# Kernel optimization log

Measured on AMD Instinct MI355X. Metric: run time of the kernel, lower is better.

## Reference

```python
import jax, jax.numpy as jnp
import numpy as np

B, S, D = 8, 2048, 512          # batch, seq_len, latent_doc_dim
E = 512                          # embedding_dim (== latent_doc_dim here by construction)
NUM_CATS, NUM_LABELS = 1024, 8192
EMB_SCALING = 1.0


def _norm_embed(m, scaling):
    # __init__ preprocessing: m -= m.mean(); m /= m.std() * scaling
    m = m - m.mean()
    return m / (m.std() * scaling)


def setup_inputs() -> dict:
    key = jax.random.key(0)
    k1, k2, k3, k4, k5, k6, k7 = jax.random.split(key, 7)
    K = jax.random.normal(k1, (B, S, D), dtype=jnp.float32)
    V = jax.random.normal(k2, (B, S, D), dtype=jnp.float32)
    code2cat_map = jax.random.randint(k3, (NUM_LABELS,), 0, NUM_CATS)
    # pretrained embedding matrices, normalized as in __init__
    Q1_w = _norm_embed(jax.random.normal(k4, (NUM_CATS, E), dtype=jnp.float32), EMB_SCALING)
    Q2_w = _norm_embed(jax.random.normal(k5, (NUM_LABELS, E), dtype=jnp.float32), EMB_SCALING)
    # Conv1d(kernel_size=1): weight [D_out=latent, D_in=embed], bias [latent]
    map_w = jax.random.normal(k6, (D, E), dtype=jnp.float32) / np.sqrt(E)
    map_b = jax.random.normal(k7, (D,), dtype=jnp.float32) * 0.01
    return {"K": K, "V": V, "code2cat_map": code2cat_map,
            "Q1_w": Q1_w, "Q2_w": Q2_w, "map_w": map_w, "map_b": map_b}


def reference(K, V, code2cat_map, Q1_w, Q2_w, map_w, map_b):
    # kernel-size-1 Conv1d mapping == affine projection of each row embedding
    Q1 = jnp.einsum('ce,de->cd', Q1_w, map_w) + map_b        # [num_cats, D]
    Q2 = jnp.einsum('le,de->ld', Q2_w, map_w) + map_b        # [num_labels, D]
    # level-1 attention (scale=False)
    E1 = jnp.einsum('cd,bsd->bcs', Q1, K)                    # [B, num_cats, S]
    A1 = jax.nn.softmax(E1, axis=-1)
    C1 = jnp.einsum('bcs,bsd->bcd', A1, V)                   # [B, num_cats, D]
    # inject level-1 context into level-2 queries via code->category gather-add
    Q2b = Q2[None, :, :] + C1[:, code2cat_map, :]            # [B, num_labels, D]
    # level-2 attention
    E2 = jnp.einsum('bld,bsd->bls', Q2b, K)                  # [B, num_labels, S]
    A2 = jax.nn.softmax(E2, axis=-1)
    C2 = jnp.einsum('bls,bsd->bld', A2, V)                   # [B, num_labels, D]
    return (C2, E2)
```

## Files before the change

### kernel.cpp

```cpp
#include <hip/hip_runtime.h>
#include <hip/hip_bf16.h>
#include <stdint.h>

#define BB 8
#define SS 2048
#define DD 512
#define NCAT 1024
#define NLAB 8192

typedef short bf16x8 __attribute__((ext_vector_type(8)));
typedef short bf16x4_t __attribute__((ext_vector_type(4)));
typedef float f32x4 __attribute__((ext_vector_type(4)));

#define BAR() do { asm volatile("" ::: "memory"); __builtin_amdgcn_s_barrier(); asm volatile("" ::: "memory"); } while (0)

__device__ __forceinline__ unsigned short f2bf(float f) {
  union { float f; unsigned int u; } v; v.f = f;
  unsigned int u = v.u;
  return (unsigned short)((u + 0x7fffu + ((u >> 16) & 1u)) >> 16);
}
__device__ __forceinline__ float bf2f(unsigned short h) {
  union { unsigned int u; float f; } v; v.u = ((unsigned int)h) << 16;
  return v.f;
}

__device__ __forceinline__ void gload_lds16(const void* g, void* l) {
  __builtin_amdgcn_global_load_lds(
      (const __attribute__((address_space(1))) unsigned int*)g,
      (__attribute__((address_space(3))) unsigned int*)l, 16, 0, 0);
}

__global__ __launch_bounds__(512, 2) void gemm_e2(
    const short* __restrict__ A,
    const short* __restrict__ Bm,
    float* __restrict__ E2, float* __restrict__ pm, float* __restrict__ ps)
{
  __shared__ __align__(16) char lds[3 * 32768];
  const int t = threadIdx.x;
  const int w = t >> 6, lane = t & 63;
  const int r = lane & 15, g = lane >> 4;
  const int wm = w >> 2, wn = w & 3;
  const int m0 = blockIdx.x * 256, n0 = blockIdx.y * 256;
  const int b = blockIdx.z;
  const short* Ab = A + (long)b * NLAB * DD;
  const short* Bb = Bm + (long)b * SS * DD;

  int offA[8], offB[4];
#pragma unroll
  for (int i = 0; i < 8; ++i) {
    int row = wm * 128 + i * 16 + r;
    int grp = row >> 1, slot = ((row & 1) << 2) | g;
    offA[i] = grp * 128 + (slot ^ (grp & 7)) * 16;
  }
#pragma unroll
  for (int j = 0; j < 4; ++j) {
    int row = wn * 64 + j * 16 + r;
    int grp = row >> 1, slot = ((row & 1) << 2) | g;
    offB[j] = grp * 128 + (slot ^ (grp & 7)) * 16;
  }

  int srow[2], scol[2];
#pragma unroll
  for (int ld = 0; ld < 2; ++ld) {
    int ch = ld * 512 + t;
    int grp = ch >> 3, sl2 = (ch & 7) ^ (grp & 7);
    srow[ld] = grp * 2 + (sl2 >> 2);
    scol[ld] = (sl2 & 3) * 8;
  }

  auto stageA = [&](int kt, int buf) {
    const long kb = (long)(kt * 32);
#pragma unroll
    for (int ld = 0; ld < 2; ++ld)
      gload_lds16(Ab + (long)(m0 + srow[ld]) * DD + kb + scol[ld],
                  lds + buf * 32768 + (ld * 512 + t) * 16);
  };
  auto stageB = [&](int kt, int buf) {
    const long kb = (long)(kt * 32);
#pragma unroll
    for (int ld = 0; ld < 2; ++ld)
      gload_lds16(Bb + (long)(n0 + srow[ld]) * DD + kb + scol[ld],
                  lds + buf * 32768 + 16384 + (ld * 512 + t) * 16);
  };

  f32x4 acc[8][4] = {};

  stageA(0, 0); stageB(0, 0);
  stageA(1, 1); stageB(1, 1);
  asm volatile("s_waitcnt vmcnt(4)" ::: "memory");
  BAR();

  int cur = 0;
#pragma unroll 1
  for (int kt = 0; kt < 16; ++kt) {
    const char* bA = lds + cur * 32768;
    const char* bB = bA + 16384;
    const int nxt = (cur == 0) ? 2 : cur - 1;

    bf16x8 av[4], av2[4], bv[4];
#pragma unroll
    for (int j = 0; j < 4; ++j) bv[j] = *(const bf16x8*)(bB + offB[j]);
#pragma unroll
    for (int i = 0; i < 4; ++i) av[i] = *(const bf16x8*)(bA + offA[i]);
    if (kt + 2 < 16) stageA(kt + 2, nxt);
    BAR();
    __builtin_amdgcn_s_setprio(1);
#pragma unroll
    for (int i = 0; i < 4; ++i)
#pragma unroll
      for (int j = 0; j < 4; ++j)
        acc[i][j] = __builtin_amdgcn_mfma_f32_16x16x32_bf16(av[i], bv[j], acc[i][j], 0, 0, 0);
    __builtin_amdgcn_s_setprio(0);
    BAR();
#pragma unroll
    for (int i = 0; i < 4; ++i) av2[i] = *(const bf16x8*)(bA + offA[4 + i]);
    if (kt + 2 < 16) stageB(kt + 2, nxt);
    BAR();
    __builtin_amdgcn_s_setprio(1);
#pragma unroll
    for (int i = 0; i < 4; ++i)
#pragma unroll
      for (int j = 0; j < 4; ++j)
        acc[4 + i][j] = __builtin_amdgcn_mfma_f32_16x16x32_bf16(av2[i], bv[j], acc[4 + i][j], 0, 0, 0);
    __builtin_amdgcn_s_setprio(0);
    if (kt < 15) {
      if (kt == 14) asm volatile("s_waitcnt vmcnt(0)" ::: "memory");
      else          asm volatile("s_waitcnt vmcnt(4)" ::: "memory");
    }
    BAR();
    cur = (cur == 2) ? 0 : cur + 1;
  }

  float* Cg = E2 + (long)b * NLAB * SS;
#pragma unroll
  for (int i = 0; i < 8; ++i)
#pragma unroll
    for (int j = 0; j < 4; ++j) {
      const int col = n0 + wn * 64 + j * 16 + r;
#pragma unroll
      for (int q = 0; q < 4; ++q) {
        const int row = m0 + wm * 128 + i * 16 + g * 4 + q;
        Cg[(long)row * SS + col] = acc[i][j][q];
      }
    }

  BAR();

  float* smax = (float*)lds;
  float* ssum = (float*)(lds + 4096);
#pragma unroll
  for (int i = 0; i < 8; ++i)
#pragma unroll
    for (int q = 0; q < 4; ++q) {
      float mm = fmaxf(fmaxf(acc[i][0][q], acc[i][1][q]),
                       fmaxf(acc[i][2][q], acc[i][3][q]));
#pragma unroll
      for (int off = 1; off <= 8; off <<= 1) mm = fmaxf(mm, __shfl_xor(mm, off, 64));
      float s = 0.f;
#pragma unroll
      for (int j = 0; j < 4; ++j) s += __expf(acc[i][j][q] - mm);
#pragma unroll
      for (int off = 1; off <= 8; off <<= 1) s += __shfl_xor(s, off, 64);
      if (r == 0) {
        const int rowt = wm * 128 + i * 16 + g * 4 + q;
        smax[rowt * 4 + wn] = mm;
        ssum[rowt * 4 + wn] = s;
      }
    }
  BAR();
  if (t < 256) {
    float m0_ = smax[t * 4 + 0], m1_ = smax[t * 4 + 1];
    float m2_ = smax[t * 4 + 2], m3_ = smax[t * 4 + 3];
    float mm = fmaxf(fmaxf(m0_, m1_), fmaxf(m2_, m3_));
    float s = ssum[t * 4 + 0] * __expf(m0_ - mm) + ssum[t * 4 + 1] * __expf(m1_ - mm)
            + ssum[t * 4 + 2] * __expf(m2_ - mm) + ssum[t * 4 + 3] * __expf(m3_ - mm);
    const long base = ((long)b * NLAB + m0 + t) * 8 + (n0 >> 8);
    pm[base] = mm;
    ps[base] = s;
  }
}

__global__ __launch_bounds__(512, 2) void gemm_c2p(
    const float* __restrict__ E2, const float2* __restrict__ stats,
    const short* __restrict__ VT, float* __restrict__ C2)
{
  __shared__ __align__(16) char lds[3 * 32768];
  const int t = threadIdx.x;
  const int w = t >> 6, lane = t & 63;
  const int r = lane & 15, g = lane >> 4;
  const int wm = w >> 2, wn = w & 3;
  const int m0 = blockIdx.x * 256, n0 = blockIdx.y * 256;
  const int b = blockIdx.z;
  const float* Eb = E2 + (long)b * NLAB * SS;
  const short* Bb = VT + (long)b * DD * SS;

  int offA[8], offB[4];
#pragma unroll
  for (int i = 0; i < 8; ++i) {
    int row = wm * 128 + i * 16 + r;
    int grp = row >> 1, slot = ((row & 1) << 2) | g;
    offA[i] = grp * 128 + (slot ^ (grp & 7)) * 16;
  }
#pragma unroll
  for (int j = 0; j < 4; ++j) {
    int row = wn * 64 + j * 16 + r;
    int grp = row >> 1, slot = ((row & 1) << 2) | g;
    offB[j] = grp * 128 + (slot ^ (grp & 7)) * 16;
  }

  int srow[2], scol[2];
#pragma unroll
  for (int ld = 0; ld < 2; ++ld) {
    int ch = ld * 512 + t;
    int grp = ch >> 3, sl2 = (ch & 7) ^ (grp & 7);
    srow[ld] = grp * 2 + (sl2 >> 2);
    scol[ld] = (sl2 & 3) * 8;
  }

  const int arow = t >> 1;
  const int ac0 = (t & 1) * 16;
  int wbyte[2];
  {
    const int grp = arow >> 1, cc0 = ac0 >> 3;
#pragma unroll
    for (int ld = 0; ld < 2; ++ld) {
      const int slot = ((arow & 1) << 2) | (cc0 + ld);
      wbyte[ld] = grp * 128 + (slot ^ (grp & 7)) * 16;
    }
  }
  const float2 st = stats[(long)b * NLAB + m0 + arow];
  const float* asrc = Eb + (long)(m0 + arow) * SS + ac0;

  float areg[16];
  auto loadA = [&](int kt) {
    const float* src = asrc + kt * 32;
#pragma unroll
    for (int u = 0; u < 4; ++u)
      *(f32x4*)(areg + u * 4) = *(const f32x4*)(src + u * 4);
  };
  auto writeA = [&](int buf) {
    char* dst = lds + buf * 32768;
#pragma unroll
    for (int ld = 0; ld < 2; ++ld) {
      bf16x8 p;
#pragma unroll
      for (int q = 0; q < 8; ++q)
        p[q] = (short)f2bf(__expf(areg[ld * 8 + q] - st.x) * st.y);
      *(bf16x8*)(dst + wbyte[ld]) = p;
    }
  };
  auto stageB = [&](int kt, int buf) {
    const long kb = (long)(kt * 32);
#pragma unroll
    for (int ld = 0; ld < 2; ++ld)
      gload_lds16(Bb + (long)(n0 + srow[ld]) * SS + kb + scol[ld],
                  lds + buf * 32768 + 16384 + (ld * 512 + t) * 16);
  };

  f32x4 acc[8][4] = {};

  loadA(0); stageB(0, 0); writeA(0);
  loadA(1); stageB(1, 1); writeA(1);
  asm volatile("s_waitcnt lgkmcnt(0)" ::: "memory");
  BAR();

  int cur = 0;
#pragma unroll 1
  for (int kt = 0; kt < 64; ++kt) {
    const char* bA = lds + cur * 32768;
    const char* bB = bA + 16384;
    const int nxt = (cur == 0) ? 2 : cur - 1;

    bf16x8 av[4], av2[4], bv[4];
#pragma unroll
    for (int j = 0; j < 4; ++j) bv[j] = *(const bf16x8*)(bB + offB[j]);
#pragma unroll
    for (int i = 0; i < 4; ++i) av[i] = *(const bf16x8*)(bA + offA[i]);
    if (kt + 2 < 64) loadA(kt + 2);
    BAR();
    __builtin_amdgcn_s_setprio(1);
#pragma unroll
    for (int i = 0; i < 4; ++i)
#pragma unroll
      for (int j = 0; j < 4; ++j)
        acc[i][j] = __builtin_amdgcn_mfma_f32_16x16x32_bf16(av[i], bv[j], acc[i][j], 0, 0, 0);
    __builtin_amdgcn_s_setprio(0);
    BAR();
#pragma unroll
    for (int i = 0; i < 4; ++i) av2[i] = *(const bf16x8*)(bA + offA[4 + i]);
    if (kt + 2 < 64) stageB(kt + 2, nxt);
    BAR();
    __builtin_amdgcn_s_setprio(1);
#pragma unroll
    for (int i = 0; i < 4; ++i)
#pragma unroll
      for (int j = 0; j < 4; ++j)
        acc[4 + i][j] = __builtin_amdgcn_mfma_f32_16x16x32_bf16(av2[i], bv[j], acc[4 + i][j], 0, 0, 0);
    __builtin_amdgcn_s_setprio(0);
    if (kt + 2 < 64) writeA(nxt);
    if (kt == 62) asm volatile("s_waitcnt vmcnt(0)" ::: "memory");
    asm volatile("s_waitcnt lgkmcnt(0)" ::: "memory");
    BAR();
    cur = (cur == 2) ? 0 : cur + 1;
  }

  float* Cg = C2 + (long)b * NLAB * DD;
#pragma unroll
  for (int i = 0; i < 8; ++i)
#pragma unroll
    for (int j = 0; j < 4; ++j) {
      const int col = n0 + wn * 64 + j * 16 + r;
#pragma unroll
      for (int q = 0; q < 4; ++q) {
        const int row = m0 + wm * 128 + i * 16 + g * 4 + q;
        Cg[(long)row * DD + col] = acc[i][j][q];
      }
    }
}

template<int BIAS, int TERMS>
__global__ __launch_bounds__(256) void gemm_nt_split(
    const short* __restrict__ Ah, const short* __restrict__ Al,
    const short* __restrict__ Bh, const short* __restrict__ Bl,
    float* __restrict__ C, const float* __restrict__ bias,
    int M, int N, int K, long sA, long sB, long sC)
{
  __shared__ short AsH[128 * 32];
  __shared__ short AsL[TERMS == 3 ? 128 * 32 : 8];
  __shared__ short BsH[128 * 32];
  __shared__ short BsL[TERMS == 3 ? 128 * 32 : 8];
  const int t = threadIdx.x, w = t >> 6, l = t & 63;
  const int r = l & 15, g = l >> 4;
  const int m0 = blockIdx.x * 128, n0 = blockIdx.y * 128;
  const int b = blockIdx.z;
  const short* Ahb = Ah + (long)b * sA;
  const short* Alb = TERMS == 3 ? Al + (long)b * sA : (const short*)0;
  const short* Bhb = Bh + (long)b * sB;
  const short* Blb = TERMS == 3 ? Bl + (long)b * sB : (const short*)0;
  float* Cg = C + (long)b * sC;
  const int wm = (w >> 1) * 64, wn = (w & 1) * 64;
  const int srow = t >> 2, scol = (t & 3) * 8;

  f32x4 acc[4][4] = {};

  const int nk = K >> 5;
  for (int kt = 0; kt < nk; ++kt) {
    const long k0 = (long)(kt << 5);
    const long ga0 = (long)(m0 + srow) * K + k0 + scol;
    const long ga1 = (long)(m0 + srow + 64) * K + k0 + scol;
    const long gb0 = (long)(n0 + srow) * K + k0 + scol;
    const long gb1 = (long)(n0 + srow + 64) * K + k0 + scol;
    gload_lds16(Ahb + ga0, &AsH[w * 512]);
    gload_lds16(Ahb + ga1, &AsH[2048 + w * 512]);
    gload_lds16(Bhb + gb0, &BsH[w * 512]);
    gload_lds16(Bhb + gb1, &BsH[2048 + w * 512]);
    if (TERMS == 3) {
      gload_lds16(Alb + ga0, &AsL[w * 512]);
      gload_lds16(Alb + ga1, &AsL[2048 + w * 512]);
      gload_lds16(Blb + gb0, &BsL[w * 512]);
      gload_lds16(Blb + gb1, &BsL[2048 + w * 512]);
    }
    __syncthreads();
    bf16x8 ah[4], al_[4], bh[4], bl_[4];
#pragma unroll
    for (int i = 0; i < 4; ++i) {
      ah[i]  = *(const bf16x8*)&AsH[(wm + i * 16 + r) * 32 + g * 8];
      bh[i]  = *(const bf16x8*)&BsH[(wn + i * 16 + r) * 32 + g * 8];
      if (TERMS == 3) {
        al_[i] = *(const bf16x8*)&AsL[(wm + i * 16 + r) * 32 + g * 8];
        bl_[i] = *(const bf16x8*)&BsL[(wn + i * 16 + r) * 32 + g * 8];
      }
    }
#pragma unroll
    for (int i = 0; i < 4; ++i)
#pragma unroll
      for (int j = 0; j < 4; ++j) {
        if (TERMS == 3) {
          acc[i][j] = __builtin_amdgcn_mfma_f32_16x16x32_bf16(al_[i], bh[j], acc[i][j], 0, 0, 0);
          acc[i][j] = __builtin_amdgcn_mfma_f32_16x16x32_bf16(ah[i], bl_[j], acc[i][j], 0, 0, 0);
        }
        acc[i][j] = __builtin_amdgcn_mfma_f32_16x16x32_bf16(ah[i], bh[j], acc[i][j], 0, 0, 0);
      }
    __syncthreads();
  }

#pragma unroll
  for (int i = 0; i < 4; ++i)
#pragma unroll
    for (int j = 0; j < 4; ++j) {
      f32x4 v = acc[i][j];
      const int col = n0 + wn + j * 16 + r;
      float bv = 0.f;
      if (BIAS) bv = bias[col];
#pragma unroll
      for (int q = 0; q < 4; ++q) {
        const int row = m0 + wm + i * 16 + g * 4 + q;
        Cg[(long)row * N + col] = v[q] + bv;
      }
    }
}

__global__ __launch_bounds__(256) void stats_combine(
    const float* __restrict__ pm, const float* __restrict__ ps,
    float2* __restrict__ stats)
{
  const long row = (long)blockIdx.x * 256 + threadIdx.x;
  const float* m = pm + row * 8;
  const float* s = ps + row * 8;
  float mv[8];
  float mm = -3.4e38f;
#pragma unroll
  for (int j = 0; j < 8; ++j) { mv[j] = m[j]; mm = fmaxf(mm, mv[j]); }
  float ss = 0.f;
#pragma unroll
  for (int j = 0; j < 8; ++j) ss += s[j] * __expf(mv[j] - mm);
  stats[row] = make_float2(mm, 1.f / ss);
}

__global__ __launch_bounds__(256) void rowsoft_p(
    const float* __restrict__ X, short* __restrict__ Ph)
{
  __shared__ float red[8];
  const long row = blockIdx.x;
  const float* x = X + row * SS;
  const int t = threadIdx.x, w = t >> 6;
  f32x4 v0 = *(const f32x4*)(x + t * 4);
  f32x4 v1 = *(const f32x4*)(x + 1024 + t * 4);
  float m = fmaxf(fmaxf(fmaxf(v0[0], v0[1]), fmaxf(v0[2], v0[3])),
                  fmaxf(fmaxf(v1[0], v1[1]), fmaxf(v1[2], v1[3])));
#pragma unroll
  for (int off = 32; off; off >>= 1) m = fmaxf(m, __shfl_xor(m, off, 64));
  if ((t & 63) == 0) red[w] = m;
  __syncthreads();
  m = fmaxf(fmaxf(red[0], red[1]), fmaxf(red[2], red[3]));
  float s = 0.f;
#pragma unroll
  for (int i = 0; i < 4; ++i) { v0[i] = __expf(v0[i] - m); s += v0[i]; }
#pragma unroll
  for (int i = 0; i < 4; ++i) { v1[i] = __expf(v1[i] - m); s += v1[i]; }
#pragma unroll
  for (int off = 32; off; off >>= 1) s += __shfl_xor(s, off, 64);
  if ((t & 63) == 0) red[4 + w] = s;
  __syncthreads();
  s = red[4] + red[5] + red[6] + red[7];
  const float inv = 1.f / s;
  bf16x4_t h0, h1;
#pragma unroll
  for (int i = 0; i < 4; ++i) {
    h0[i] = (short)f2bf(v0[i] * inv);
    h1[i] = (short)f2bf(v1[i] * inv);
  }
  *(bf16x4_t*)(Ph + row * SS + t * 4) = h0;
  *(bf16x4_t*)(Ph + row * SS + 1024 + t * 4) = h1;
}

__global__ __launch_bounds__(256) void cvt_split(
    const float* __restrict__ in, short* __restrict__ hi, short* __restrict__ lo, long n4)
{
  long i = (long)blockIdx.x * 256 + threadIdx.x;
  const long stride = (long)gridDim.x * 256;
  for (; i < n4; i += stride) {
    f32x4 v = *(const f32x4*)(in + i * 4);
    bf16x4_t h, lw;
#pragma unroll
    for (int q = 0; q < 4; ++q) {
      h[q] = (short)f2bf(v[q]);
      lw[q] = (short)f2bf(v[q] - bf2f((unsigned short)h[q]));
    }
    *(bf16x4_t*)(hi + i * 4) = h;
    *(bf16x4_t*)(lo + i * 4) = lw;
  }
}

__global__ __launch_bounds__(256) void vtrans(
    const float* __restrict__ V, short* __restrict__ TH)
{
  __shared__ float tile[32][33];
  const int b = blockIdx.z;
  const int s0 = blockIdx.x * 32, d0 = blockIdx.y * 32;
  const int tx = threadIdx.x & 31, ty = threadIdx.x >> 5;
  const float* Vb = V + (long)b * SS * DD;
  short* Hb = TH + (long)b * DD * SS;
#pragma unroll
  for (int i = 0; i < 32; i += 8)
    tile[ty + i][tx] = Vb[(long)(s0 + ty + i) * DD + d0 + tx];
  __syncthreads();
#pragma unroll
  for (int i = 0; i < 32; i += 8)
    Hb[(long)(d0 + ty + i) * SS + s0 + tx] = (short)f2bf(tile[tx][ty + i]);
}

__global__ __launch_bounds__(256) void make_q2b(
    const float* __restrict__ Q2f, const float* __restrict__ C1,
    const int* __restrict__ map, short* __restrict__ Oh)
{
  const long idx = (long)blockIdx.x * 256 + threadIdx.x;
  const long per_b = (long)NLAB * (DD / 4);
  const int b = (int)(idx / per_b);
  const long rem = idx - (long)b * per_b;
  const int ll = (int)(rem >> 7);
  const int dd = (int)(rem & 127) << 2;
  const int cat = map[ll];
  f32x4 qv = *(const f32x4*)(Q2f + (long)ll * DD + dd);
  f32x4 cv = *(const f32x4*)(C1 + ((long)b * NCAT + cat) * DD + dd);
  bf16x4_t h;
#pragma unroll
  for (int q = 0; q < 4; ++q) h[q] = (short)f2bf(qv[q] + cv[q]);
  *(bf16x4_t*)(Oh + idx * 4) = h;
}

extern "C" void kernel_launch(void* const* d_in, const int* in_sizes, int n_in,
                              void* d_out, int out_size, void* d_ws, size_t ws_size,
                              hipStream_t stream)
{
  const float* K    = (const float*)d_in[0];
  const float* V    = (const float*)d_in[1];
  const int*   map  = (const int*)d_in[2];
  const float* Q1w  = (const float*)d_in[3];
  const float* Q2w  = (const float*)d_in[4];
  const float* mapw = (const float*)d_in[5];
  const float* mapb = (const float*)d_in[6];

  float* out = (float*)d_out;
  const long C2SZ = (long)BB * NLAB * DD;
  float* outC2 = out;
  float* outE2 = out + C2SZ;

  char* ws = (char*)d_ws;
  short* Kh   = (short*)ws; ws += (long)BB * SS * DD * 2;
  short* Kl   = (short*)ws; ws += (long)BB * SS * DD * 2;
  short* VTh  = (short*)ws; ws += (long)BB * DD * SS * 2;
  short* Qwh  = (short*)ws; ws += (long)(NCAT + NLAB) * DD * 2;
  short* Qwl  = (short*)ws; ws += (long)(NCAT + NLAB) * DD * 2;
  short* mwh  = (short*)ws; ws += (long)DD * DD * 2;
  short* mwl  = (short*)ws; ws += (long)DD * DD * 2;
  float* Qall = (float*)ws; ws += (long)(NCAT + NLAB) * DD * 4;
  short* A1h  = (short*)ws; ws += (long)BB * NCAT * SS * 2;
  float* C1   = (float*)ws; ws += (long)BB * NCAT * DD * 4;
  short* Q2bh = (short*)ws; ws += (long)BB * NLAB * DD * 2;
  float* pm   = (float*)ws; ws += (long)BB * NLAB * 8 * 4;
  float* psum = (float*)ws; ws += (long)BB * NLAB * 8 * 4;
  float2* stats = (float2*)ws;

  cvt_split<<<2048, 256, 0, stream>>>(K, Kh, Kl, (long)BB * SS * DD / 4);
  vtrans<<<dim3(SS / 32, DD / 32, BB), 256, 0, stream>>>(V, VTh);
  cvt_split<<<512, 256, 0, stream>>>(Q1w, Qwh, Qwl, (long)NCAT * DD / 4);
  cvt_split<<<2048, 256, 0, stream>>>(Q2w, Qwh + (long)NCAT * DD, Qwl + (long)NCAT * DD,
                                      (long)NLAB * DD / 4);
  cvt_split<<<256, 256, 0, stream>>>(mapw, mwh, mwl, (long)DD * DD / 4);

  gemm_nt_split<1, 3><<<dim3((NCAT + NLAB) / 128, DD / 128, 1), 256, 0, stream>>>(
      Qwh, Qwl, mwh, mwl, Qall, mapb, NCAT + NLAB, DD, DD, 0, 0, 0);

  cvt_split<<<2048, 256, 0, stream>>>(Qall, Qwh, Qwl, (long)(NCAT + NLAB) * DD / 4);

  gemm_nt_split<0, 3><<<dim3(NCAT / 128, SS / 128, BB), 256, 0, stream>>>(
      Qwh, Qwl, Kh, Kl, outE2, (const float*)0,
      NCAT, SS, DD, 0, (long)SS * DD, (long)NCAT * SS);

  rowsoft_p<<<BB * NCAT, 256, 0, stream>>>(outE2, A1h);

  gemm_nt_split<0, 1><<<dim3(NCAT / 128, DD / 128, BB), 256, 0, stream>>>(
      A1h, (const short*)0, VTh, (const short*)0, C1, (const float*)0,
      NCAT, DD, SS, (long)NCAT * SS, (long)DD * SS, (long)NCAT * DD);

  make_q2b<<<(int)((long)BB * NLAB * DD / 4 / 256), 256, 0, stream>>>(
      Qall + (long)NCAT * DD, C1, map, Q2bh);

  gemm_e2<<<dim3(NLAB / 256, SS / 256, BB), 512, 0, stream>>>(
      Q2bh, Kh, outE2, pm, psum);

  stats_combine<<<BB * NLAB / 256, 256, 0, stream>>>(pm, psum, stats);

  gemm_c2p<<<dim3(NLAB / 256, DD / 256, BB), 512, 0, stream>>>(
      outE2, stats, VTh, outC2);
}
```

Measured before the change: 794.8 us.

## Reuse tuned QK and PV kernels for level-1 attention via concatenated split-bf16 operands

Level-1 attention now uses the pipelined 256x256 gemm_qk and gemm_pv kernels. The 3-term split-bf16 product is expressed as a single GEMM with K=1536 over concatenated [Qh|Ql|Qh] and [Kh|Kl|Kh] operands. The separate Qall split-conversion pass and the rowsoft_p kernel are removed. Softmax stats are fused into the QK epilogue and normalization into the PV kernel, and the Q1 split is written straight from the projection GEMM epilogue. This trades extra Kcat workspace and conversion writes for fewer launches, no materialized A1, and better-tuned GEMMs.

```diff
diff --git a/kernel.cpp b/kernel.cpp
--- a/kernel.cpp
+++ b/kernel.cpp
@@ -30,11 +30,15 @@
       (__attribute__((address_space(3))) unsigned int*)l, 16, 0, 0);
 }
 
-__global__ __launch_bounds__(512, 2) void gemm_e2(
-    const short* __restrict__ A,
-    const short* __restrict__ Bm,
-    float* __restrict__ E2, float* __restrict__ pm, float* __restrict__ ps)
-{
+template<int KK>
+__global__ __launch_bounds__(512, 2) void gemm_qk(
+    const short* __restrict__ A, long sA,
+    const short* __restrict__ Bc,
+    float* __restrict__ E, float* __restrict__ pm, float* __restrict__ ps,
+    int M)
+{
+  constexpr int NK = KK / 32;
+  constexpr int AS = (KK == 512) ? 512 : 1024;
   __shared__ __align__(16) char lds[3 * 32768];
   const int t = threadIdx.x;
   const int w = t >> 6, lane = t & 63;
@@ -42,8 +46,8 @@
   const int wm = w >> 2, wn = w & 3;
   const int m0 = blockIdx.x * 256, n0 = blockIdx.y * 256;
   const int b = blockIdx.z;
-  const short* Ab = A + (long)b * NLAB * DD;
-  const short* Bb = Bm + (long)b * SS * DD;
+  const short* Ab = A + (long)b * sA;
+  const short* Bb = Bc + (long)b * SS * KK;
 
   int offA[8], offB[4];
 #pragma unroll
@@ -69,17 +73,18 @@
   }
 
   auto stageA = [&](int kt, int buf) {
-    const long kb = (long)(kt * 32);
+    const int ab = (KK == 512) ? kt : (kt < 32 ? (kt & 15) : (kt - 16));
+    const long kb = (long)ab * 32;
 #pragma unroll
     for (int ld = 0; ld < 2; ++ld)
-      gload_lds16(Ab + (long)(m0 + srow[ld]) * DD + kb + scol[ld],
+      gload_lds16(Ab + (long)(m0 + srow[ld]) * AS + kb + scol[ld],
                   lds + buf * 32768 + (ld * 512 + t) * 16);
   };
   auto stageB = [&](int kt, int buf) {
     const long kb = (long)(kt * 32);
 #pragma unroll
     for (int ld = 0; ld < 2; ++ld)
-      gload_lds16(Bb + (long)(n0 + srow[ld]) * DD + kb + scol[ld],
+      gload_lds16(Bb + (long)(n0 + srow[ld]) * KK + kb + scol[ld],
                   lds + buf * 32768 + 16384 + (ld * 512 + t) * 16);
   };
 
@@ -92,7 +97,7 @@
 
   int cur = 0;
 #pragma unroll 1
-  for (int kt = 0; kt < 16; ++kt) {
+  for (int kt = 0; kt < NK; ++kt) {
     const char* bA = lds + cur * 32768;
     const char* bB = bA + 16384;
     const int nxt = (cur == 0) ? 2 : cur - 1;
@@ -102,7 +107,7 @@
     for (int j = 0; j < 4; ++j) bv[j] = *(const bf16x8*)(bB + offB[j]);
 #pragma unroll
     for (int i = 0; i < 4; ++i) av[i] = *(const bf16x8*)(bA + offA[i]);
-    if (kt + 2 < 16) stageA(kt + 2, nxt);
+    if (kt + 2 < NK) stageA(kt + 2, nxt);
     BAR();
     __builtin_amdgcn_s_setprio(1);
 #pragma unroll
@@ -114,7 +119,7 @@
     BAR();
 #pragma unroll
     for (int i = 0; i < 4; ++i) av2[i] = *(const bf16x8*)(bA + offA[4 + i]);
-    if (kt + 2 < 16) stageB(kt + 2, nxt);
+    if (kt + 2 < NK) stageB(kt + 2, nxt);
     BAR();
     __builtin_amdgcn_s_setprio(1);
 #pragma unroll
@@ -123,15 +128,15 @@
       for (int j = 0; j < 4; ++j)
         acc[4 + i][j] = __builtin_amdgcn_mfma_f32_16x16x32_bf16(av2[i], bv[j], acc[4 + i][j], 0, 0, 0);
     __builtin_amdgcn_s_setprio(0);
-    if (kt < 15) {
-      if (kt == 14) asm volatile("s_waitcnt vmcnt(0)" ::: "memory");
-      else          asm volatile("s_waitcnt vmcnt(4)" ::: "memory");
+    if (kt < NK - 1) {
+      if (kt == NK - 2) asm volatile("s_waitcnt vmcnt(0)" ::: "memory");
+      else              asm volatile("s_waitcnt vmcnt(4)" ::: "memory");
     }
     BAR();
     cur = (cur == 2) ? 0 : cur + 1;
   }
 
-  float* Cg = E2 + (long)b * NLAB * SS;
+  float* Cg = E + (long)b * M * SS;
 #pragma unroll
   for (int i = 0; i < 8; ++i)
 #pragma unroll
@@ -174,15 +179,15 @@
     float mm = fmaxf(fmaxf(m0_, m1_), fmaxf(m2_, m3_));
     float s = ssum[t * 4 + 0] * __expf(m0_ - mm) + ssum[t * 4 + 1] * __expf(m1_ - mm)
             + ssum[t * 4 + 2] * __expf(m2_ - mm) + ssum[t * 4 + 3] * __expf(m3_ - mm);
-    const long base = ((long)b * NLAB + m0 + t) * 8 + (n0 >> 8);
+    const long base = ((long)b * M + m0 + t) * 8 + (n0 >> 8);
     pm[base] = mm;
     ps[base] = s;
   }
 }
 
-__global__ __launch_bounds__(512, 2) void gemm_c2p(
-    const float* __restrict__ E2, const float2* __restrict__ stats,
-    const short* __restrict__ VT, float* __restrict__ C2)
+__global__ __launch_bounds__(512, 2) void gemm_pv(
+    const float* __restrict__ E, const float2* __restrict__ stats,
+    const short* __restrict__ VT, float* __restrict__ C, int M)
 {
   __shared__ __align__(16) char lds[3 * 32768];
   const int t = threadIdx.x;
@@ -191,7 +196,7 @@
   const int wm = w >> 2, wn = w & 3;
   const int m0 = blockIdx.x * 256, n0 = blockIdx.y * 256;
   const int b = blockIdx.z;
-  const float* Eb = E2 + (long)b * NLAB * SS;
+  const float* Eb = E + (long)b * M * SS;
   const short* Bb = VT + (long)b * DD * SS;
 
   int offA[8], offB[4];
@@ -228,7 +233,7 @@
       wbyte[ld] = grp * 128 + (slot ^ (grp & 7)) * 16;
     }
   }
-  const float2 st = stats[(long)b * NLAB + m0 + arow];
+  const float2 st = stats[(long)b * M + m0 + arow];
   const float* asrc = Eb + (long)(m0 + arow) * SS + ac0;
 
   float areg[16];
@@ -304,7 +309,7 @@
     cur = (cur == 2) ? 0 : cur + 1;
   }
 
-  float* Cg = C2 + (long)b * NLAB * DD;
+  float* Cg = C + (long)b * M * DD;
 #pragma unroll
   for (int i = 0; i < 8; ++i)
 #pragma unroll
@@ -318,26 +323,20 @@
     }
 }
 
-template<int BIAS, int TERMS>
+template<int BIAS, int WQCAT>
 __global__ __launch_bounds__(256) void gemm_nt_split(
     const short* __restrict__ Ah, const short* __restrict__ Al,
     const short* __restrict__ Bh, const short* __restrict__ Bl,
-    float* __restrict__ C, const float* __restrict__ bias,
-    int M, int N, int K, long sA, long sB, long sC)
+    float* __restrict__ C, short* __restrict__ Qcat, const float* __restrict__ bias,
+    int M, int N, int K)
 {
   __shared__ short AsH[128 * 32];
-  __shared__ short AsL[TERMS == 3 ? 128 * 32 : 8];
+  __shared__ short AsL[128 * 32];
   __shared__ short BsH[128 * 32];
-  __shared__ short BsL[TERMS == 3 ? 128 * 32 : 8];
+  __shared__ short BsL[128 * 32];
   const int t = threadIdx.x, w = t >> 6, l = t & 63;
   const int r = l & 15, g = l >> 4;
   const int m0 = blockIdx.x * 128, n0 = blockIdx.y * 128;
-  const int b = blockIdx.z;
-  const short* Ahb = Ah + (long)b * sA;
-  const short* Alb = TERMS == 3 ? Al + (long)b * sA : (const short*)0;
-  const short* Bhb = Bh + (long)b * sB;
-  const short* Blb = TERMS == 3 ? Bl + (long)b * sB : (const short*)0;
-  float* Cg = C + (long)b * sC;
   const int wm = (w >> 1) * 64, wn = (w & 1) * 64;
   const int srow = t >> 2, scol = (t & 3) * 8;
 
@@ -350,35 +349,29 @@
     const long ga1 = (long)(m0 + srow + 64) * K + k0 + scol;
     const long gb0 = (long)(n0 + srow) * K + k0 + scol;
     const long gb1 = (long)(n0 + srow + 64) * K + k0 + scol;
-    gload_lds16(Ahb + ga0, &AsH[w * 512]);
-    gload_lds16(Ahb + ga1, &AsH[2048 + w * 512]);
-    gload_lds16(Bhb + gb0, &BsH[w * 512]);
-    gload_lds16(Bhb + gb1, &BsH[2048 + w * 512]);
-    if (TERMS == 3) {
-      gload_lds16(Alb + ga0, &AsL[w * 512]);
-      gload_lds16(Alb + ga1, &AsL[2048 + w * 512]);
-      gload_lds16(Blb + gb0, &BsL[w * 512]);
-      gload_lds16(Blb + gb1, &BsL[2048 + w * 512]);
-    }
+    gload_lds16(Ah + ga0, &AsH[w * 512]);
+    gload_lds16(Ah + ga1, &AsH[2048 + w * 512]);
+    gload_lds16(Bh + gb0, &BsH[w * 512]);
+    gload_lds16(Bh + gb1, &BsH[2048 + w * 512]);
+    gload_lds16(Al + ga0, &AsL[w * 512]);
+    gload_lds16(Al + ga1, &AsL[2048 + w * 512]);
+    gload_lds16(Bl + gb0, &BsL[w * 512]);
+    gload_lds16(Bl + gb1, &BsL[2048 + w * 512]);
     __syncthreads();
     bf16x8 ah[4], al_[4], bh[4], bl_[4];
 #pragma unroll
     for (int i = 0; i < 4; ++i) {
       ah[i]  = *(const bf16x8*)&AsH[(wm + i * 16 + r) * 32 + g * 8];
       bh[i]  = *(const bf16x8*)&BsH[(wn + i * 16 + r) * 32 + g * 8];
-      if (TERMS == 3) {
-        al_[i] = *(const bf16x8*)&AsL[(wm + i * 16 + r) * 32 + g * 8];
-        bl_[i] = *(const bf16x8*)&BsL[(wn + i * 16 + r) * 32 + g * 8];
-      }
+      al_[i] = *(const bf16x8*)&AsL[(wm + i * 16 + r) * 32 + g * 8];
+      bl_[i] = *(const bf16x8*)&BsL[(wn + i * 16 + r) * 32 + g * 8];
     }
 #pragma unroll
     for (int i = 0; i < 4; ++i)
 #pragma unroll
       for (int j = 0; j < 4; ++j) {
-        if (TERMS == 3) {
-          acc[i][j] = __builtin_amdgcn_mfma_f32_16x16x32_bf16(al_[i], bh[j], acc[i][j], 0, 0, 0);
-          acc[i][j] = __builtin_amdgcn_mfma_f32_16x16x32_bf16(ah[i], bl_[j], acc[i][j], 0, 0, 0);
-        }
+        acc[i][j] = __builtin_amdgcn_mfma_f32_16x16x32_bf16(al_[i], bh[j], acc[i][j], 0, 0, 0);
+        acc[i][j] = __builtin_amdgcn_mfma_f32_16x16x32_bf16(ah[i], bl_[j], acc[i][j], 0, 0, 0);
         acc[i][j] = __builtin_amdgcn_mfma_f32_16x16x32_bf16(ah[i], bh[j], acc[i][j], 0, 0, 0);
       }
     __syncthreads();
@@ -395,7 +388,13 @@
 #pragma unroll
       for (int q = 0; q < 4; ++q) {
         const int row = m0 + wm + i * 16 + g * 4 + q;
-        Cg[(long)row * N + col] = v[q] + bv;
+        const float val = v[q] + bv;
+        C[(long)row * N + col] = val;
+        if (WQCAT && row < NCAT) {
+          unsigned short h = f2bf(val);
+          Qcat[(long)row * 1024 + col] = (short)h;
+          Qcat[(long)row * 1024 + 512 + col] = (short)f2bf(val - bf2f(h));
+        }
       }
     }
 }
@@ -417,43 +416,6 @@
   stats[row] = make_float2(mm, 1.f / ss);
 }
 
-__global__ __launch_bounds__(256) void rowsoft_p(
-    const float* __restrict__ X, short* __restrict__ Ph)
-{
-  __shared__ float red[8];
-  const long row = blockIdx.x;
-  const float* x = X + row * SS;
-  const int t = threadIdx.x, w = t >> 6;
-  f32x4 v0 = *(const f32x4*)(x + t * 4);
-  f32x4 v1 = *(const f32x4*)(x + 1024 + t * 4);
-  float m = fmaxf(fmaxf(fmaxf(v0[0], v0[1]), fmaxf(v0[2], v0[3])),
-                  fmaxf(fmaxf(v1[0], v1[1]), fmaxf(v1[2], v1[3])));
-#pragma unroll
-  for (int off = 32; off; off >>= 1) m = fmaxf(m, __shfl_xor(m, off, 64));
-  if ((t & 63) == 0) red[w] = m;
-  __syncthreads();
-  m = fmaxf(fmaxf(red[0], red[1]), fmaxf(red[2], red[3]));
-  float s = 0.f;
-#pragma unroll
-  for (int i = 0; i < 4; ++i) { v0[i] = __expf(v0[i] - m); s += v0[i]; }
-#pragma unroll
-  for (int i = 0; i < 4; ++i) { v1[i] = __expf(v1[i] - m); s += v1[i]; }
-#pragma unroll
-  for (int off = 32; off; off >>= 1) s += __shfl_xor(s, off, 64);
-  if ((t & 63) == 0) red[4 + w] = s;
-  __syncthreads();
-  s = red[4] + red[5] + red[6] + red[7];
-  const float inv = 1.f / s;
-  bf16x4_t h0, h1;
-#pragma unroll
-  for (int i = 0; i < 4; ++i) {
-    h0[i] = (short)f2bf(v0[i] * inv);
-    h1[i] = (short)f2bf(v1[i] * inv);
-  }
-  *(bf16x4_t*)(Ph + row * SS + t * 4) = h0;
-  *(bf16x4_t*)(Ph + row * SS + 1024 + t * 4) = h1;
-}
-
 __global__ __launch_bounds__(256) void cvt_split(
     const float* __restrict__ in, short* __restrict__ hi, short* __restrict__ lo, long n4)
 {
@@ -470,6 +432,26 @@
     *(bf16x4_t*)(hi + i * 4) = h;
     *(bf16x4_t*)(lo + i * 4) = lw;
   }
+}
+
+__global__ __launch_bounds__(256) void cvt_kcat(
+    const float* __restrict__ K, short* __restrict__ Kh, short* __restrict__ Kcat)
+{
+  const long i = (long)blockIdx.x * 256 + threadIdx.x;
+  f32x4 v = *(const f32x4*)(K + i * 4);
+  bf16x4_t h, lw;
+#pragma unroll
+  for (int q = 0; q < 4; ++q) {
+    h[q] = (short)f2bf(v[q]);
+    lw[q] = (short)f2bf(v[q] - bf2f((unsigned short)h[q]));
+  }
+  *(bf16x4_t*)(Kh + i * 4) = h;
+  const long srow = i >> 7;
+  const int c = (int)(i & 127) * 4;
+  short* rowp = Kcat + srow * 1536;
+  *(bf16x4_t*)(rowp + c) = h;
+  *(bf16x4_t*)(rowp + 512 + c) = lw;
+  *(bf16x4_t*)(rowp + 1024 + c) = h;
 }
 
 __global__ __launch_bounds__(256) void vtrans(
@@ -527,51 +509,48 @@
   float* outE2 = out + C2SZ;
 
   char* ws = (char*)d_ws;
-  short* Kh   = (short*)ws; ws += (long)BB * SS * DD * 2;
-  short* Kl   = (short*)ws; ws += (long)BB * SS * DD * 2;
-  short* VTh  = (short*)ws; ws += (long)BB * DD * SS * 2;
-  short* Qwh  = (short*)ws; ws += (long)(NCAT + NLAB) * DD * 2;
-  short* Qwl  = (short*)ws; ws += (long)(NCAT + NLAB) * DD * 2;
-  short* mwh  = (short*)ws; ws += (long)DD * DD * 2;
-  short* mwl  = (short*)ws; ws += (long)DD * DD * 2;
-  float* Qall = (float*)ws; ws += (long)(NCAT + NLAB) * DD * 4;
-  short* A1h  = (short*)ws; ws += (long)BB * NCAT * SS * 2;
-  float* C1   = (float*)ws; ws += (long)BB * NCAT * DD * 4;
-  short* Q2bh = (short*)ws; ws += (long)BB * NLAB * DD * 2;
-  float* pm   = (float*)ws; ws += (long)BB * NLAB * 8 * 4;
-  float* psum = (float*)ws; ws += (long)BB * NLAB * 8 * 4;
-  float2* stats = (float2*)ws;
-
-  cvt_split<<<2048, 256, 0, stream>>>(K, Kh, Kl, (long)BB * SS * DD / 4);
+  short* Kh    = (short*)ws; ws += (long)BB * SS * DD * 2;
+  short* Kcat  = (short*)ws; ws += (long)BB * SS * 1536 * 2;
+  short* VTh   = (short*)ws; ws += (long)BB * DD * SS * 2;
+  short* Qwh   = (short*)ws; ws += (long)(NCAT + NLAB) * DD * 2;
+  short* Qwl   = (short*)ws; ws += (long)(NCAT + NLAB) * DD * 2;
+  short* mwh   = (short*)ws; ws += (long)DD * DD * 2;
+  short* mwl   = (short*)ws; ws += (long)DD * DD * 2;
+  float* Qall  = (float*)ws; ws += (long)(NCAT + NLAB) * DD * 4;
+  short* Qcat  = (short*)ws; ws += (long)NCAT * 1024 * 2;
+  float* C1    = (float*)ws; ws += (long)BB * NCAT * DD * 4;
+  short* Q2bh  = (short*)ws; ws += (long)BB * NLAB * DD * 2;
+  float* pm    = (float*)ws; ws += (long)BB * NLAB * 8 * 4;
+  float* psum  = (float*)ws; ws += (long)BB * NLAB * 8 * 4;
+  float* pm1   = (float*)ws; ws += (long)BB * NCAT * 8 * 4;
+  float* ps1   = (float*)ws; ws += (long)BB * NCAT * 8 * 4;
+  float2* stats  = (float2*)ws; ws += (long)BB * NLAB * 8;
+  float2* stats1 = (float2*)ws;
+
+  cvt_kcat<<<(int)((long)BB * SS * DD / 4 / 256), 256, 0, stream>>>(K, Kh, Kcat);
   vtrans<<<dim3(SS / 32, DD / 32, BB), 256, 0, stream>>>(V, VTh);
   cvt_split<<<512, 256, 0, stream>>>(Q1w, Qwh, Qwl, (long)NCAT * DD / 4);
   cvt_split<<<2048, 256, 0, stream>>>(Q2w, Qwh + (long)NCAT * DD, Qwl + (long)NCAT * DD,
                                       (long)NLAB * DD / 4);
   cvt_split<<<256, 256, 0, stream>>>(mapw, mwh, mwl, (long)DD * DD / 4);
 
-  gemm_nt_split<1, 3><<<dim3((NCAT + NLAB) / 128, DD / 128, 1), 256, 0, stream>>>(
-      Qwh, Qwl, mwh, mwl, Qall, mapb, NCAT + NLAB, DD, DD, 0, 0, 0);
-
-  cvt_split<<<2048, 256, 0, stream>>>(Qall, Qwh, Qwl, (long)(NCAT + NLAB) * DD / 4);
-
-  gemm_nt_split<0, 3><<<dim3(NCAT / 128, SS / 128, BB), 256, 0, stream>>>(
-      Qwh, Qwl, Kh, Kl, outE2, (const float*)0,
-      NCAT, SS, DD, 0, (long)SS * DD, (long)NCAT * SS);
-
-  rowsoft_p<<<BB * NCAT, 256, 0, stream>>>(outE2, A1h);
-
-  gemm_nt_split<0, 1><<<dim3(NCAT / 128, DD / 128, BB), 256, 0, stream>>>(
-      A1h, (const short*)0, VTh, (const short*)0, C1, (const float*)0,
-      NCAT, DD, SS, (long)NCAT * SS, (long)DD * SS, (long)NCAT * DD);
+  gemm_nt_split<1, 1><<<dim3((NCAT + NLAB) / 128, DD / 128, 1), 256, 0, stream>>>(
+      Qwh, Qwl, mwh, mwl, Qall, Qcat, mapb, NCAT + NLAB, DD, DD);
+
+  gemm_qk<1536><<<dim3(NCAT / 256, SS / 256, BB), 512, 0, stream>>>(
+      Qcat, 0L, Kcat, outE2, pm1, ps1, NCAT);
+  stats_combine<<<BB * NCAT / 256, 256, 0, stream>>>(pm1, ps1, stats1);
+
+  gemm_pv<<<dim3(NCAT / 256, DD / 256, BB), 512, 0, stream>>>(
+      outE2, stats1, VTh, C1, NCAT);
 
   make_q2b<<<(int)((long)BB * NLAB * DD / 4 / 256), 256, 0, stream>>>(
       Qall + (long)NCAT * DD, C1, map, Q2bh);
 
-  gemm_e2<<<dim3(NLAB / 256, SS / 256, BB), 512, 0, stream>>>(
-      Q2bh, Kh, outE2, pm, psum);
-
+  gemm_qk<512><<<dim3(NLAB / 256, SS / 256, BB), 512, 0, stream>>>(
+      Q2bh, (long)NLAB * DD, Kh, outE2, pm, psum, NLAB);
   stats_combine<<<BB * NLAB / 256, 256, 0, stream>>>(pm, psum, stats);
 
-  gemm_c2p<<<dim3(NLAB / 256, DD / 256, BB), 512, 0, stream>>>(
-      outE2, stats, VTh, outC2);
-}
+  gemm_pv<<<dim3(NLAB / 256, DD / 256, BB), 512, 0, stream>>>(
+      outE2, stats, VTh, outC2, NLAB);
+}
```

Result: slower. 829.2 us (+4.3%).
